# Kernel optimization log

Measured on AMD Instinct MI355X. Metric: run time of the kernel, lower is better.

Reference implementation:

```python
import jax, jax.numpy as jnp
import numpy as np

B = 64          # graphs per batch
N = 1500        # nodes per graph (equal sizes -> vectorized sortpool)
NT = B * N      # total nodes
DEG = 16        # avg in-degree
E_PER = N * DEG # edges per graph
F_IN = 128
K = 30          # sortpool k
LATENT = [32, 32, 32, 1]  # total 97
TOTAL_LAT = sum(LATENT)
OUT_DIM = 128


def setup_inputs() -> dict:
    key = jax.random.key(0)
    ks = jax.random.split(key, 16)
    node_feat = jax.random.normal(ks[0], (NT, F_IN), dtype=jnp.float32)
    # edges constrained within each graph (block-diagonal adjacency)
    offs = (jnp.arange(B, dtype=jnp.int32) * N)[:, None]
    edge_src = (jax.random.randint(ks[1], (B, E_PER), 0, N, dtype=jnp.int32) + offs).reshape(-1)
    edge_dst = (jax.random.randint(ks[2], (B, E_PER), 0, N, dtype=jnp.int32) + offs).reshape(-1)

    def lin(k, fan_in, shape):
        return jax.random.normal(k, shape, dtype=jnp.float32) * (1.0 / np.sqrt(fan_in))

    inp = dict(node_feat=node_feat, edge_src=edge_src, edge_dst=edge_dst)
    dims = [F_IN] + LATENT
    for i in range(4):
        inp[f'W{i+1}'] = lin(ks[3 + i], dims[i], (dims[i], dims[i + 1]))
        inp[f'b{i+1}'] = jnp.zeros((dims[i + 1],), jnp.float32)
    inp['conv1_w'] = lin(ks[8], TOTAL_LAT, (16, TOTAL_LAT))   # Conv1d(1,16,97,stride=97)
    inp['conv1_b'] = jnp.zeros((16,), jnp.float32)
    inp['conv2_w'] = lin(ks[9], 16 * 5, (32, 16, 5))          # Conv1d(16,32,5)
    inp['conv2_b'] = jnp.zeros((32,), jnp.float32)
    inp['out_w'] = lin(ks[10], 352, (352, OUT_DIM))
    inp['out_b'] = jnp.zeros((OUT_DIM,), jnp.float32)
    return inp


def reference(node_feat, edge_src, edge_dst, W1, b1, W2, b2, W3, b3, W4, b4,
              conv1_w, conv1_b, conv2_w, conv2_b, out_w, out_b):
    # node degrees (+1 for self loop), from in-edges
    deg = jax.ops.segment_sum(jnp.ones_like(edge_dst, jnp.float32), edge_dst, num_segments=NT)
    node_degs = (deg + 1.0)[:, None]

    # 4 graph-conv layers: (A @ h + h) -> Linear -> /deg -> tanh, concat features
    h = node_feat
    layers = []
    for W, b in ((W1, b1), (W2, b2), (W3, b3), (W4, b4)):
        agg = jax.ops.segment_sum(h[edge_src], edge_dst, num_segments=NT) + h
        h = jnp.tanh((agg @ W + b) / node_degs)
        layers.append(h)
    feat = jnp.concatenate(layers, axis=1)  # [NT, 97]

    # sortpooling: top-k nodes per graph by the last channel
    sort_ch = feat[:, -1].reshape(B, N)
    _, idx = jax.lax.top_k(sort_ch, K)                    # [B, K]
    gidx = (idx + (jnp.arange(B, dtype=idx.dtype) * N)[:, None]).reshape(-1)
    pooled = feat[gidx].reshape(B, K, TOTAL_LAT)          # [B, K, 97]

    # Conv1d(1,16,97,stride=97) over flattened [B,1,K*97] == per-slot linear
    c1 = jax.nn.relu(jnp.einsum('bkd,od->bok', pooled, conv1_w) + conv1_b[None, :, None])  # [B,16,K]
    mp = c1.reshape(B, 16, K // 2, 2).max(axis=-1)        # MaxPool1d(2,2) -> [B,16,15]
    c2 = jax.lax.conv_general_dilated(mp, conv2_w, (1,), 'VALID',
                                      dimension_numbers=('NCH', 'OIH', 'NCH'))
    c2 = jax.nn.relu(c2 + conv2_b[None, :, None])         # [B,32,11]
    dense = c2.reshape(B, -1)                             # [B,352]
    return jax.nn.relu(dense @ out_w + out_b)             # relu(relu(x)) == relu(x)
```

## Files before the change

### kernel.cpp

```cpp
#include <hip/hip_runtime.h>

constexpr int B = 64, N = 1500, NT = B * N;
constexpr int E_PER = 24000, E_TOT = B * E_PER;
constexpr int E_PAD = 28512;
constexpr int F_INN = 128, K = 30, TOT = 97;
constexpr int NB_G = 47;

__global__ __launch_bounds__(1024) void build_csr(const int* __restrict__ src, const int* __restrict__ dst,
                                                  int* __restrict__ csr, int* __restrict__ rowst,
                                                  int* __restrict__ degi, float* __restrict__ degf,
                                                  float* __restrict__ tA, float* __restrict__ tB,
                                                  float* __restrict__ t4) {
    __shared__ int hist[N];
    __shared__ int csr_l[E_PAD];
    __shared__ int wsum[4];
    int g = blockIdx.x, t = threadIdx.x;
    int gbase = g * N;
    const int* dstg = dst + (size_t)g * E_PER;
    const int* srcg = src + (size_t)g * E_PER;

    if (g == 0) {
        if (t < 32) tA[(size_t)NT * 32 + t] = 0.f;
        else if (t < 64) tB[(size_t)NT * 32 + (t - 32)] = 0.f;
        else if (t == 64) t4[NT] = 0.f;
    }

    for (int i = t; i < N; i += 1024) hist[i] = 0;
    for (int i = t; i < E_PAD; i += 1024) csr_l[i] = NT;
    __syncthreads();
    for (int e = t; e < E_PER; e += 1024)
        atomicAdd(&hist[dstg[e] - gbase], 1);
    __syncthreads();

    int local[6];
    int sum = 0, x = 0;
    if (t < 256) {
#pragma unroll
        for (int i = 0; i < 6; ++i) {
            int v = t * 6 + i;
            int d = (v < N) ? hist[v] : 0;
            local[i] = d;
            sum += (d + 3) & ~3;
        }
        x = sum;
        int lane = t & 63;
#pragma unroll
        for (int m = 1; m < 64; m <<= 1) {
            int y = __shfl_up(x, m, 64);
            if (lane >= m) x += y;
        }
        if (lane == 63) wsum[t >> 6] = x;
    }
    __syncthreads();
    if (t < 256) {
        int woff = 0;
        int wv = t >> 6;
        for (int w = 0; w < wv; ++w) woff += wsum[w];
        int run = x - sum + woff;
#pragma unroll
        for (int i = 0; i < 6; ++i) {
            int v = t * 6 + i;
            if (v < N) {
                rowst[gbase + v] = g * E_PAD + run;
                degi[gbase + v] = local[i];
                degf[gbase + v] = (float)(local[i] + 1);
                hist[v] = run;
                run += (local[i] + 3) & ~3;
            }
        }
    }
    __syncthreads();
    for (int e = t; e < E_PER; e += 1024) {
        int d = dstg[e] - gbase;
        int pos = atomicAdd(&hist[d], 1);
        csr_l[pos] = srcg[e];
    }
    __syncthreads();
    for (int i = t; i < E_PAD; i += 1024)
        csr[(size_t)g * E_PAD + i] = csr_l[i];
}

template <int KDIM>
__global__ __launch_bounds__(256) void gemm_t(const float* __restrict__ h,
                                              const float* __restrict__ W,
                                              float* __restrict__ t) {
    __shared__ float hs[32][128];
    __shared__ float Ws[32][32];
    int tid = threadIdx.x;
    int wv = tid >> 6, lane = tid & 63;
    int v0 = blockIdx.x * 128;
    int og = wv * 8;
    float acc[2][8];
#pragma unroll
    for (int i = 0; i < 2; ++i)
#pragma unroll
        for (int j = 0; j < 8; ++j) acc[i][j] = 0.f;

    for (int kc = 0; kc < KDIM; kc += 32) {
        __syncthreads();
        {
            int n = tid >> 1, kh = (tid & 1) * 16;
            const float* hp = h + (size_t)(v0 + n) * KDIM + kc + kh;
            const float4* hp4 = reinterpret_cast<const float4*>(hp);
            float4 a = hp4[0], b = hp4[1], c = hp4[2], d = hp4[3];
            hs[kh + 0][n] = a.x;  hs[kh + 1][n] = a.y;  hs[kh + 2][n] = a.z;  hs[kh + 3][n] = a.w;
            hs[kh + 4][n] = b.x;  hs[kh + 5][n] = b.y;  hs[kh + 6][n] = b.z;  hs[kh + 7][n] = b.w;
            hs[kh + 8][n] = c.x;  hs[kh + 9][n] = c.y;  hs[kh + 10][n] = c.z; hs[kh + 11][n] = c.w;
            hs[kh + 12][n] = d.x; hs[kh + 13][n] = d.y; hs[kh + 14][n] = d.z; hs[kh + 15][n] = d.w;
        }
        {
            int r = tid >> 3, c4 = (tid & 7) * 4;
            float4 w = *reinterpret_cast<const float4*>(W + (size_t)(kc + r) * 32 + c4);
            *reinterpret_cast<float4*>(&Ws[r][c4]) = w;
        }
        __syncthreads();
#pragma unroll
        for (int k = 0; k < 32; ++k) {
            float2 hv = *reinterpret_cast<const float2*>(&hs[k][2 * lane]);
            float4 w0 = *reinterpret_cast<const float4*>(&Ws[k][og]);
            float4 w1 = *reinterpret_cast<const float4*>(&Ws[k][og + 4]);
            acc[0][0] += hv.x * w0.x; acc[0][1] += hv.x * w0.y; acc[0][2] += hv.x * w0.z; acc[0][3] += hv.x * w0.w;
            acc[0][4] += hv.x * w1.x; acc[0][5] += hv.x * w1.y; acc[0][6] += hv.x * w1.z; acc[0][7] += hv.x * w1.w;
            acc[1][0] += hv.y * w0.x; acc[1][1] += hv.y * w0.y; acc[1][2] += hv.y * w0.z; acc[1][3] += hv.y * w0.w;
            acc[1][4] += hv.y * w1.x; acc[1][5] += hv.y * w1.y; acc[1][6] += hv.y * w1.z; acc[1][7] += hv.y * w1.w;
        }
    }
#pragma unroll
    for (int i = 0; i < 2; ++i) {
        float* op = t + (size_t)(v0 + 2 * lane + i) * 32 + og;
        float4 r0 = {acc[i][0], acc[i][1], acc[i][2], acc[i][3]};
        float4 r1 = {acc[i][4], acc[i][5], acc[i][6], acc[i][7]};
        reinterpret_cast<float4*>(op)[0] = r0;
        reinterpret_cast<float4*>(op)[1] = r1;
    }
}

template <int FUSE>
__global__ __launch_bounds__(256) void agg_f(const float* __restrict__ t,
                                             const int* __restrict__ csr, const int* __restrict__ rowst,
                                             const int* __restrict__ degi, const float* __restrict__ degf,
                                             const float* __restrict__ bias, const float* __restrict__ Wn,
                                             float* __restrict__ hout, float* __restrict__ tn) {
    __shared__ float Ws[1024];
    __shared__ float outs[32][32];
    if (FUSE == 32) {
        for (int i = threadIdx.x; i < 1024; i += 256) Ws[i] = Wn[i];
    }
    int bid = blockIdx.x;
    int xcd = bid & 7, j = bid >> 3;
    int g = xcd + 8 * (j / NB_G);
    int nb = j % NB_G;
    int nl = threadIdx.x >> 3;
    int f4 = threadIdx.x & 7;
    int vl = nb * 32 + nl;
    bool valid = vl < N;
    int v = g * N + vl;
    const float4* t4v = reinterpret_cast<const float4*>(t);
    float4 out = {0.f, 0.f, 0.f, 0.f};
    if (valid) {
        float4 acc = t4v[(unsigned)(v * 8 + f4)];
        int e0 = rowst[v];
        int dc = degi[v];
        int pc = (dc + 3) & ~3;
        float4 s1 = {0.f, 0.f, 0.f, 0.f}, s2 = {0.f, 0.f, 0.f, 0.f};
        for (int e = 0; e < pc; e += 4) {
            int4 s4 = *reinterpret_cast<const int4*>(csr + e0 + e);
            float4 x0 = t4v[(unsigned)(s4.x * 8 + f4)];
            float4 x1 = t4v[(unsigned)(s4.y * 8 + f4)];
            float4 x2 = t4v[(unsigned)(s4.z * 8 + f4)];
            float4 x3 = t4v[(unsigned)(s4.w * 8 + f4)];
            s1.x += x0.x + x1.x; s1.y += x0.y + x1.y; s1.z += x0.z + x1.z; s1.w += x0.w + x1.w;
            s2.x += x2.x + x3.x; s2.y += x2.y + x3.y; s2.z += x2.z + x3.z; s2.w += x2.w + x3.w;
        }
        acc.x += s1.x + s2.x; acc.y += s1.y + s2.y; acc.z += s1.z + s2.z; acc.w += s1.w + s2.w;
        float4 bv = *reinterpret_cast<const float4*>(bias + f4 * 4);
        float inv = 1.0f / degf[v];
        out.x = tanhf((acc.x + bv.x) * inv);
        out.y = tanhf((acc.y + bv.y) * inv);
        out.z = tanhf((acc.z + bv.z) * inv);
        out.w = tanhf((acc.w + bv.w) * inv);
        reinterpret_cast<float4*>(hout)[(unsigned)(v * 8 + f4)] = out;
    }
    if (FUSE == 32) {
        *reinterpret_cast<float4*>(&outs[nl][f4 * 4]) = out;
        __syncthreads();
        if (valid) {
            float4 s = {0.f, 0.f, 0.f, 0.f};
#pragma unroll
            for (int ff = 0; ff < 32; ++ff) {
                float h = outs[nl][ff];
                float4 wr = *reinterpret_cast<const float4*>(&Ws[ff * 32 + f4 * 4]);
                s.x += h * wr.x; s.y += h * wr.y; s.z += h * wr.z; s.w += h * wr.w;
            }
            reinterpret_cast<float4*>(tn)[(unsigned)(v * 8 + f4)] = s;
        }
    } else if (valid) {
        float4 w4 = *reinterpret_cast<const float4*>(Wn + f4 * 4);
        float p = out.x * w4.x + out.y * w4.y + out.z * w4.z + out.w * w4.w;
        p += __shfl_xor(p, 4, 64);
        p += __shfl_xor(p, 2, 64);
        p += __shfl_xor(p, 1, 64);
        if (f4 == 0) tn[v] = p;
    }
}

__global__ __launch_bounds__(256) void agg1f(const float* __restrict__ t4,
                                             const int* __restrict__ csr, const int* __restrict__ rowst,
                                             const int* __restrict__ degi, const float* __restrict__ degf,
                                             const float* __restrict__ b4, float* __restrict__ h4) {
    int v = blockIdx.x * 256 + threadIdx.x;
    if (v >= NT) return;
    float acc = t4[v];
    int e0 = rowst[v], dc = degi[v];
    int pc = (dc + 3) & ~3;
    float a0 = 0.f, a1 = 0.f, a2 = 0.f, a3 = 0.f;
    for (int e = 0; e < pc; e += 4) {
        int4 s4 = *reinterpret_cast<const int4*>(csr + e0 + e);
        a0 += t4[s4.x];
        a1 += t4[s4.y];
        a2 += t4[s4.z];
        a3 += t4[s4.w];
    }
    acc += (a0 + a1) + (a2 + a3);
    h4[v] = tanhf((acc + b4[0]) / degf[v]);
}

__global__ __launch_bounds__(512) void sort_head(const float* __restrict__ hc1, const float* __restrict__ hc2,
                                                 const float* __restrict__ hc3, const float* __restrict__ h4,
                                                 const float* __restrict__ c1w, const float* __restrict__ c1b,
                                                 const float* __restrict__ c2w, const float* __restrict__ c2b,
                                                 const float* __restrict__ ow, const float* __restrict__ ob,
                                                 float* __restrict__ out) {
    __shared__ unsigned int svals[N];
    __shared__ float fvals[N];
    __shared__ int hist[2048];
    __shared__ int canA[N], canB[N];
    __shared__ int winners[32];
    __shared__ int wsum[8];
    __shared__ int st_need, st_ncand, st_tb, st_cab, st_nwin;
    __shared__ int topk_s[K];
    __shared__ float pooled[K][TOT];
    __shared__ float c1[16][K];
    __shared__ float mp[16][16];
    __shared__ float dense[352];
    __shared__ float part[4][128];

    int g = blockIdx.x, t = threadIdx.x;
    int gbase = g * N;
    int lane = t & 63, w = t >> 6;

    for (int v = t; v < N; v += 512) {
        float f = h4[gbase + v];
        fvals[v] = f;
        unsigned int b = __float_as_uint(f);
        svals[v] = (b & 0x80000000u) ? ~b : (b | 0x80000000u);
    }
    if (t == 0) { st_need = K; st_nwin = 0; }

    auto mkkey = [&](int idx) {
        return ((unsigned long long)svals[idx] << 31) | (unsigned int)(0x7FFFFFFF - idx);
    };

    const int SHIFTS[6] = {52, 41, 30, 19, 8, 0};
    int curN = N;
    int src = 0;
    for (int pass = 0; pass < 6; ++pass) {
        int shift = SHIFTS[pass];
        int mask = (pass == 5) ? 0xFF : 0x7FF;
        for (int i = t; i < 2048; i += 512) hist[i] = 0;
        if (t == 0) st_ncand = 0;
        __syncthreads();
        for (int i = t; i < curN; i += 512) {
            int idx = (src == 0) ? i : (src == 1 ? canA[i] : canB[i]);
            int d = (int)((mkkey(idx) >> shift) & mask);
            atomicAdd(&hist[d], 1);
        }
        __syncthreads();
        int need = st_need;
        int c[4];
        int s = 0;
#pragma unroll
        for (int u = 0; u < 4; ++u) { c[u] = hist[2047 - (4 * t + u)]; s += c[u]; }
        int x = s;
#pragma unroll
        for (int m = 1; m < 64; m <<= 1) {
            int y = __shfl_up(x, m, 64);
            if (lane >= m) x += y;
        }
        if (lane == 63) wsum[w] = x;
        __syncthreads();
        int woff = 0;
        for (int ww = 0; ww < w; ++ww) woff += wsum[ww];
        int A = woff + x - s;
#pragma unroll
        for (int u = 0; u < 4; ++u) {
            if (A < need && need <= A + c[u]) { st_tb = 2047 - (4 * t + u); st_cab = A; }
            A += c[u];
        }
        __syncthreads();
        int tb = st_tb, cab = st_cab;
        int* dst = (src == 1) ? canB : canA;
        for (int i = t; i < curN; i += 512) {
            int idx = (src == 0) ? i : (src == 1 ? canA[i] : canB[i]);
            int d = (int)((mkkey(idx) >> shift) & mask);
            if (d > tb) {
                int p = atomicAdd(&st_nwin, 1);
                winners[p] = idx;
            } else if (d == tb) {
                int p = atomicAdd(&st_ncand, 1);
                dst[p] = idx;
            }
        }
        __syncthreads();
        int ncand = st_ncand;
        need -= cab;
        if (t == 0) st_need = need;
        if (ncand == need) {
            int base = st_nwin;
            for (int i = t; i < ncand; i += 512) winners[base + i] = dst[i];
            __syncthreads();
            break;
        }
        curN = ncand;
        src = (src == 1) ? 2 : 1;
        __syncthreads();
    }

    if (t < 64) {
        unsigned long long key = (t < K) ? mkkey(winners[t]) : 0ull;
        unsigned long long kk = ~key;
#pragma unroll
        for (int k = 2; k <= 64; k <<= 1) {
#pragma unroll
            for (int j = k >> 1; j > 0; j >>= 1) {
                unsigned long long o = __shfl_xor(kk, j, 64);
                bool keepMin = ((t & j) == 0) == ((t & k) == 0);
                kk = keepMin ? (kk < o ? kk : o) : (kk > o ? kk : o);
            }
        }
        key = ~kk;
        if (t < K) topk_s[t] = 0x7FFFFFFF - (int)(unsigned int)(key & 0x7FFFFFFFu);
    }
    __syncthreads();

    for (int i = t; i < K * TOT; i += 512) {
        int k = i / TOT, d = i % TOT;
        int vloc = topk_s[k];
        int gi = gbase + vloc;
        float val = (d < 32) ? hc1[(size_t)gi * 32 + d]
                  : (d < 64) ? hc2[(size_t)gi * 32 + d - 32]
                  : (d < 96) ? hc3[(size_t)gi * 32 + d - 64]
                             : fvals[vloc];
        pooled[k][d] = val;
    }
    __syncthreads();
    for (int i = t; i < 16 * K; i += 512) {
        int o = i / K, k = i % K;
        float s = c1b[o];
        for (int d = 0; d < TOT; ++d) s += pooled[k][d] * c1w[o * TOT + d];
        c1[o][k] = fmaxf(s, 0.f);
    }
    __syncthreads();
    for (int i = t; i < 16 * 15; i += 512) {
        int o = i / 15, p = i % 15;
        mp[o][p] = fmaxf(c1[o][2 * p], c1[o][2 * p + 1]);
    }
    __syncthreads();
    for (int i = t; i < 352; i += 512) {
        int o = i / 11, p = i % 11;
        float s = c2b[o];
#pragma unroll
        for (int ci = 0; ci < 16; ++ci)
#pragma unroll
            for (int tt = 0; tt < 5; ++tt)
                s += mp[ci][p + tt] * c2w[(o * 16 + ci) * 5 + tt];
        dense[i] = fmaxf(s, 0.f);
    }
    __syncthreads();
    {
        int o = t & 127, q = t >> 7;
        float s = 0.f;
        for (int m = q * 88; m < (q + 1) * 88; ++m) s += dense[m] * ow[m * 128 + o];
        part[q][o] = s;
    }
    __syncthreads();
    if (t < 128) {
        float s = (part[0][t] + part[1][t]) + (part[2][t] + part[3][t]) + ob[t];
        out[g * 128 + t] = fmaxf(s, 0.f);
    }
}

extern "C" void kernel_launch(void* const* d_in, const int* in_sizes, int n_in,
                              void* d_out, int out_size, void* d_ws, size_t ws_size,
                              hipStream_t stream) {
    const float* node_feat = (const float*)d_in[0];
    const int* esrc = (const int*)d_in[1];
    const int* edst = (const int*)d_in[2];
    const float* W1 = (const float*)d_in[3];
    const float* b1 = (const float*)d_in[4];
    const float* W2 = (const float*)d_in[5];
    const float* b2 = (const float*)d_in[6];
    const float* W3 = (const float*)d_in[7];
    const float* b3 = (const float*)d_in[8];
    const float* W4 = (const float*)d_in[9];
    const float* b4 = (const float*)d_in[10];
    const float* c1w = (const float*)d_in[11];
    const float* c1b = (const float*)d_in[12];
    const float* c2w = (const float*)d_in[13];
    const float* c2b = (const float*)d_in[14];
    const float* ow = (const float*)d_in[15];
    const float* ob = (const float*)d_in[16];

    char* ws = (char*)d_ws;
    size_t off = 0;
    auto alloc = [&](size_t bytes) {
        size_t r = off;
        off += (bytes + 255) & ~(size_t)255;
        return r;
    };
    int* deg_i = (int*)(ws + alloc((size_t)NT * 4));
    int* rowst = (int*)(ws + alloc((size_t)NT * 4));
    float* degf = (float*)(ws + alloc((size_t)NT * 4));
    int* csr = (int*)(ws + alloc((size_t)B * E_PAD * 4));
    float* tA = (float*)(ws + alloc((size_t)(NT + 1) * 32 * 4));
    float* tB = (float*)(ws + alloc((size_t)(NT + 1) * 32 * 4));
    float* hc1 = (float*)(ws + alloc((size_t)NT * 32 * 4));
    float* hc2 = (float*)(ws + alloc((size_t)NT * 32 * 4));
    float* hc3 = (float*)(ws + alloc((size_t)NT * 32 * 4));
    float* t4 = (float*)(ws + alloc((size_t)(NT + 1) * 4));
    float* h4 = (float*)(ws + alloc((size_t)NT * 4));

    build_csr<<<B, 1024, 0, stream>>>(esrc, edst, csr, rowst, deg_i, degf, tA, tB, t4);

    gemm_t<F_INN><<<NT / 128, 256, 0, stream>>>(node_feat, W1, tA);
    agg_f<32><<<8 * NB_G * 8, 256, 0, stream>>>(tA, csr, rowst, deg_i, degf, b1, W2, hc1, tB);
    agg_f<32><<<8 * NB_G * 8, 256, 0, stream>>>(tB, csr, rowst, deg_i, degf, b2, W3, hc2, tA);
    agg_f<1><<<8 * NB_G * 8, 256, 0, stream>>>(tA, csr, rowst, deg_i, degf, b3, W4, hc3, t4);
    agg1f<<<(NT + 255) / 256, 256, 0, stream>>>(t4, csr, rowst, deg_i, degf, b4, h4);

    sort_head<<<B, 512, 0, stream>>>(hc1, hc2, hc3, h4, c1w, c1b, c2w, c2b, ow, ob, (float*)d_out);
}
```

Before: 127.7 us.

## Split CSR construction across four node-quarter blocks per graph

build_csr now launches four blocks per graph instead of one. Each block owns a quarter of the destination nodes and builds its own histogram, scan and CSR slice in a smaller shared buffer (CAP=8192). The goal is to fill more of the GPU, since 64 blocks leave most CUs idle, and to cut per-block LDS use. In exchange, every block reads the full edge list of its graph, so edge reads go up fourfold. A quarter whose padded edge count exceeds CAP would overflow, though random inputs stay well below that.

```diff
diff --git a/kernel.cpp b/kernel.cpp
--- a/kernel.cpp
+++ b/kernel.cpp
@@ -2,7 +2,8 @@
 
 constexpr int B = 64, N = 1500, NT = B * N;
 constexpr int E_PER = 24000, E_TOT = B * E_PER;
-constexpr int E_PAD = 28512;
+constexpr int NQ = 4, NPQ = N / NQ;
+constexpr int CAP = 8192;
 constexpr int F_INN = 128, K = 30, TOT = 97;
 constexpr int NB_G = 47;
 
@@ -11,34 +12,38 @@
                                                   int* __restrict__ degi, float* __restrict__ degf,
                                                   float* __restrict__ tA, float* __restrict__ tB,
                                                   float* __restrict__ t4) {
-    __shared__ int hist[N];
-    __shared__ int csr_l[E_PAD];
-    __shared__ int wsum[4];
-    int g = blockIdx.x, t = threadIdx.x;
-    int gbase = g * N;
+    __shared__ int hist[NPQ];
+    __shared__ int csr_l[CAP];
+    __shared__ int wtot;
+    int bid = blockIdx.x;
+    int g = bid >> 2, q = bid & 3;
+    int t = threadIdx.x;
+    int gbase = g * N, qlo = q * NPQ;
     const int* dstg = dst + (size_t)g * E_PER;
     const int* srcg = src + (size_t)g * E_PER;
 
-    if (g == 0) {
+    if (bid == 0) {
         if (t < 32) tA[(size_t)NT * 32 + t] = 0.f;
         else if (t < 64) tB[(size_t)NT * 32 + (t - 32)] = 0.f;
         else if (t == 64) t4[NT] = 0.f;
     }
 
-    for (int i = t; i < N; i += 1024) hist[i] = 0;
-    for (int i = t; i < E_PAD; i += 1024) csr_l[i] = NT;
-    __syncthreads();
-    for (int e = t; e < E_PER; e += 1024)
-        atomicAdd(&hist[dstg[e] - gbase], 1);
-    __syncthreads();
-
-    int local[6];
+    for (int i = t; i < NPQ; i += 1024) hist[i] = 0;
+    for (int i = t; i < CAP; i += 1024) csr_l[i] = NT;
+    __syncthreads();
+    for (int e = t; e < E_PER; e += 1024) {
+        int d = dstg[e] - gbase - qlo;
+        if ((unsigned)d < (unsigned)NPQ) atomicAdd(&hist[d], 1);
+    }
+    __syncthreads();
+
+    int local[3];
     int sum = 0, x = 0;
-    if (t < 256) {
-#pragma unroll
-        for (int i = 0; i < 6; ++i) {
-            int v = t * 6 + i;
-            int d = (v < N) ? hist[v] : 0;
+    if (t < 128) {
+#pragma unroll
+        for (int i = 0; i < 3; ++i) {
+            int v = t * 3 + i;
+            int d = (v < NPQ) ? hist[v] : 0;
             local[i] = d;
             sum += (d + 3) & ~3;
         }
@@ -49,21 +54,20 @@
             int y = __shfl_up(x, m, 64);
             if (lane >= m) x += y;
         }
-        if (lane == 63) wsum[t >> 6] = x;
-    }
-    __syncthreads();
-    if (t < 256) {
-        int woff = 0;
-        int wv = t >> 6;
-        for (int w = 0; w < wv; ++w) woff += wsum[w];
-        int run = x - sum + woff;
-#pragma unroll
-        for (int i = 0; i < 6; ++i) {
-            int v = t * 6 + i;
-            if (v < N) {
-                rowst[gbase + v] = g * E_PAD + run;
-                degi[gbase + v] = local[i];
-                degf[gbase + v] = (float)(local[i] + 1);
+    }
+    if (t == 63) wtot = x;
+    __syncthreads();
+    if (t < 128) {
+        int base = (t >= 64) ? wtot : 0;
+        int run = base + x - sum;
+        int rbase = (g * NQ + q) * CAP;
+#pragma unroll
+        for (int i = 0; i < 3; ++i) {
+            int v = t * 3 + i;
+            if (v < NPQ) {
+                rowst[gbase + qlo + v] = rbase + run;
+                degi[gbase + qlo + v] = local[i];
+                degf[gbase + qlo + v] = (float)(local[i] + 1);
                 hist[v] = run;
                 run += (local[i] + 3) & ~3;
             }
@@ -71,13 +75,16 @@
     }
     __syncthreads();
     for (int e = t; e < E_PER; e += 1024) {
-        int d = dstg[e] - gbase;
-        int pos = atomicAdd(&hist[d], 1);
-        csr_l[pos] = srcg[e];
-    }
-    __syncthreads();
-    for (int i = t; i < E_PAD; i += 1024)
-        csr[(size_t)g * E_PAD + i] = csr_l[i];
+        int d = dstg[e] - gbase - qlo;
+        if ((unsigned)d < (unsigned)NPQ) {
+            int pos = atomicAdd(&hist[d], 1);
+            csr_l[pos] = srcg[e];
+        }
+    }
+    __syncthreads();
+    int* cg = csr + (size_t)(g * NQ + q) * CAP;
+    for (int i = t; i < CAP; i += 1024)
+        cg[i] = csr_l[i];
 }
 
 template <int KDIM>
@@ -421,7 +428,7 @@
     int* deg_i = (int*)(ws + alloc((size_t)NT * 4));
     int* rowst = (int*)(ws + alloc((size_t)NT * 4));
     float* degf = (float*)(ws + alloc((size_t)NT * 4));
-    int* csr = (int*)(ws + alloc((size_t)B * E_PAD * 4));
+    int* csr = (int*)(ws + alloc((size_t)B * NQ * CAP * 4));
     float* tA = (float*)(ws + alloc((size_t)(NT + 1) * 32 * 4));
     float* tB = (float*)(ws + alloc((size_t)(NT + 1) * 32 * 4));
     float* hc1 = (float*)(ws + alloc((size_t)NT * 32 * 4));
@@ -430,7 +437,7 @@
     float* t4 = (float*)(ws + alloc((size_t)(NT + 1) * 4));
     float* h4 = (float*)(ws + alloc((size_t)NT * 4));
 
-    build_csr<<<B, 1024, 0, stream>>>(esrc, edst, csr, rowst, deg_i, degf, tA, tB, t4);
+    build_csr<<<B * NQ, 1024, 0, stream>>>(esrc, edst, csr, rowst, deg_i, degf, tA, tB, t4);
 
     gemm_t<F_INN><<<NT / 128, 256, 0, stream>>>(node_feat, W1, tA);
     agg_f<32><<<8 * NB_G * 8, 256, 0, stream>>>(tA, csr, rowst, deg_i, degf, b1, W2, hc1, tB);
```

After: 129.8 us. Within noise of the previous version (+1.7%).

## Merge CSR build with first GEMM and fold last aggregation into sort_head

Applied to the files above, without the earlier changes.

Merges the CSR-building kernel and the first dense GEMM into one launch: the first B blocks build the CSR, and the remaining blocks each run four 128-node GEMM tiles in a shared-memory union. It also removes the separate scalar layer-4 aggregation kernel. sort_head now stages each graph's t4 values in LDS, gathers neighbours from there and applies tanh inline. This saves two launches and the h4 round trip through global memory. The cost is a large LDS footprint in prep, which limits occupancy for the GEMM blocks, and only 64 blocks doing the layer-4 gather.

```diff
diff --git a/kernel.cpp b/kernel.cpp
--- a/kernel.cpp
+++ b/kernel.cpp
@@ -5,133 +5,139 @@
 constexpr int E_PAD = 28512;
 constexpr int F_INN = 128, K = 30, TOT = 97;
 constexpr int NB_G = 47;
-
-__global__ __launch_bounds__(1024) void build_csr(const int* __restrict__ src, const int* __restrict__ dst,
-                                                  int* __restrict__ csr, int* __restrict__ rowst,
-                                                  int* __restrict__ degi, float* __restrict__ degf,
-                                                  float* __restrict__ tA, float* __restrict__ tB,
-                                                  float* __restrict__ t4) {
-    __shared__ int hist[N];
-    __shared__ int csr_l[E_PAD];
-    __shared__ int wsum[4];
-    int g = blockIdx.x, t = threadIdx.x;
-    int gbase = g * N;
-    const int* dstg = dst + (size_t)g * E_PER;
-    const int* srcg = src + (size_t)g * E_PER;
-
-    if (g == 0) {
-        if (t < 32) tA[(size_t)NT * 32 + t] = 0.f;
-        else if (t < 64) tB[(size_t)NT * 32 + (t - 32)] = 0.f;
-        else if (t == 64) t4[NT] = 0.f;
-    }
-
-    for (int i = t; i < N; i += 1024) hist[i] = 0;
-    for (int i = t; i < E_PAD; i += 1024) csr_l[i] = NT;
-    __syncthreads();
-    for (int e = t; e < E_PER; e += 1024)
-        atomicAdd(&hist[dstg[e] - gbase], 1);
-    __syncthreads();
-
-    int local[6];
-    int sum = 0, x = 0;
-    if (t < 256) {
-#pragma unroll
-        for (int i = 0; i < 6; ++i) {
-            int v = t * 6 + i;
-            int d = (v < N) ? hist[v] : 0;
-            local[i] = d;
-            sum += (d + 3) & ~3;
-        }
-        x = sum;
-        int lane = t & 63;
-#pragma unroll
-        for (int m = 1; m < 64; m <<= 1) {
-            int y = __shfl_up(x, m, 64);
-            if (lane >= m) x += y;
-        }
-        if (lane == 63) wsum[t >> 6] = x;
-    }
-    __syncthreads();
-    if (t < 256) {
-        int woff = 0;
-        int wv = t >> 6;
-        for (int w = 0; w < wv; ++w) woff += wsum[w];
-        int run = x - sum + woff;
-#pragma unroll
-        for (int i = 0; i < 6; ++i) {
-            int v = t * 6 + i;
-            if (v < N) {
-                rowst[gbase + v] = g * E_PAD + run;
-                degi[gbase + v] = local[i];
-                degf[gbase + v] = (float)(local[i] + 1);
-                hist[v] = run;
-                run += (local[i] + 3) & ~3;
-            }
-        }
-    }
-    __syncthreads();
-    for (int e = t; e < E_PER; e += 1024) {
-        int d = dstg[e] - gbase;
-        int pos = atomicAdd(&hist[d], 1);
-        csr_l[pos] = srcg[e];
-    }
-    __syncthreads();
-    for (int i = t; i < E_PAD; i += 1024)
-        csr[(size_t)g * E_PAD + i] = csr_l[i];
-}
-
-template <int KDIM>
-__global__ __launch_bounds__(256) void gemm_t(const float* __restrict__ h,
-                                              const float* __restrict__ W,
-                                              float* __restrict__ t) {
-    __shared__ float hs[32][128];
-    __shared__ float Ws[32][32];
-    int tid = threadIdx.x;
-    int wv = tid >> 6, lane = tid & 63;
-    int v0 = blockIdx.x * 128;
-    int og = wv * 8;
-    float acc[2][8];
-#pragma unroll
-    for (int i = 0; i < 2; ++i)
-#pragma unroll
-        for (int j = 0; j < 8; ++j) acc[i][j] = 0.f;
-
-    for (int kc = 0; kc < KDIM; kc += 32) {
-        __syncthreads();
-        {
-            int n = tid >> 1, kh = (tid & 1) * 16;
-            const float* hp = h + (size_t)(v0 + n) * KDIM + kc + kh;
-            const float4* hp4 = reinterpret_cast<const float4*>(hp);
-            float4 a = hp4[0], b = hp4[1], c = hp4[2], d = hp4[3];
-            hs[kh + 0][n] = a.x;  hs[kh + 1][n] = a.y;  hs[kh + 2][n] = a.z;  hs[kh + 3][n] = a.w;
-            hs[kh + 4][n] = b.x;  hs[kh + 5][n] = b.y;  hs[kh + 6][n] = b.z;  hs[kh + 7][n] = b.w;
-            hs[kh + 8][n] = c.x;  hs[kh + 9][n] = c.y;  hs[kh + 10][n] = c.z; hs[kh + 11][n] = c.w;
-            hs[kh + 12][n] = d.x; hs[kh + 13][n] = d.y; hs[kh + 14][n] = d.z; hs[kh + 15][n] = d.w;
-        }
-        {
-            int r = tid >> 3, c4 = (tid & 7) * 4;
-            float4 w = *reinterpret_cast<const float4*>(W + (size_t)(kc + r) * 32 + c4);
-            *reinterpret_cast<float4*>(&Ws[r][c4]) = w;
-        }
-        __syncthreads();
-#pragma unroll
-        for (int k = 0; k < 32; ++k) {
-            float2 hv = *reinterpret_cast<const float2*>(&hs[k][2 * lane]);
-            float4 w0 = *reinterpret_cast<const float4*>(&Ws[k][og]);
-            float4 w1 = *reinterpret_cast<const float4*>(&Ws[k][og + 4]);
-            acc[0][0] += hv.x * w0.x; acc[0][1] += hv.x * w0.y; acc[0][2] += hv.x * w0.z; acc[0][3] += hv.x * w0.w;
-            acc[0][4] += hv.x * w1.x; acc[0][5] += hv.x * w1.y; acc[0][6] += hv.x * w1.z; acc[0][7] += hv.x * w1.w;
-            acc[1][0] += hv.y * w0.x; acc[1][1] += hv.y * w0.y; acc[1][2] += hv.y * w0.z; acc[1][3] += hv.y * w0.w;
-            acc[1][4] += hv.y * w1.x; acc[1][5] += hv.y * w1.y; acc[1][6] += hv.y * w1.z; acc[1][7] += hv.y * w1.w;
-        }
-    }
-#pragma unroll
-    for (int i = 0; i < 2; ++i) {
-        float* op = t + (size_t)(v0 + 2 * lane + i) * 32 + og;
-        float4 r0 = {acc[i][0], acc[i][1], acc[i][2], acc[i][3]};
-        float4 r1 = {acc[i][4], acc[i][5], acc[i][6], acc[i][7]};
-        reinterpret_cast<float4*>(op)[0] = r0;
-        reinterpret_cast<float4*>(op)[1] = r1;
+constexpr int GEMM_TILES = NT / 128;
+constexpr int GEMM_BLKS = (GEMM_TILES + 3) / 4;
+
+__global__ __launch_bounds__(1024) void prep(const int* __restrict__ src, const int* __restrict__ dst,
+                                             int* __restrict__ csr, int* __restrict__ rowst,
+                                             int* __restrict__ degi, float* __restrict__ degf,
+                                             float* __restrict__ tA, float* __restrict__ tB,
+                                             float* __restrict__ t4,
+                                             const float* __restrict__ nf, const float* __restrict__ W1) {
+    __shared__ union {
+        struct { int hist[N]; int csr_l[E_PAD]; int wsum[4]; } c;
+        struct { float hs[4][32][128]; float Ws[4][32][32]; } g;
+    } u;
+    int bid = blockIdx.x, t = threadIdx.x;
+
+    if (bid < B) {
+        int g = bid;
+        int gbase = g * N;
+        const int* dstg = dst + (size_t)g * E_PER;
+        const int* srcg = src + (size_t)g * E_PER;
+
+        if (g == 0) {
+            if (t < 32) tA[(size_t)NT * 32 + t] = 0.f;
+            else if (t < 64) tB[(size_t)NT * 32 + (t - 32)] = 0.f;
+            else if (t == 64) t4[NT] = 0.f;
+        }
+
+        for (int i = t; i < N; i += 1024) u.c.hist[i] = 0;
+        for (int i = t; i < E_PAD; i += 1024) u.c.csr_l[i] = NT;
+        __syncthreads();
+        for (int e = t; e < E_PER; e += 1024)
+            atomicAdd(&u.c.hist[dstg[e] - gbase], 1);
+        __syncthreads();
+
+        int local[6];
+        int sum = 0, x = 0;
+        if (t < 256) {
+#pragma unroll
+            for (int i = 0; i < 6; ++i) {
+                int v = t * 6 + i;
+                int d = (v < N) ? u.c.hist[v] : 0;
+                local[i] = d;
+                sum += (d + 3) & ~3;
+            }
+            x = sum;
+            int lane = t & 63;
+#pragma unroll
+            for (int m = 1; m < 64; m <<= 1) {
+                int y = __shfl_up(x, m, 64);
+                if (lane >= m) x += y;
+            }
+            if (lane == 63) u.c.wsum[t >> 6] = x;
+        }
+        __syncthreads();
+        if (t < 256) {
+            int woff = 0;
+            int wv = t >> 6;
+            for (int w = 0; w < wv; ++w) woff += u.c.wsum[w];
+            int run = x - sum + woff;
+#pragma unroll
+            for (int i = 0; i < 6; ++i) {
+                int v = t * 6 + i;
+                if (v < N) {
+                    rowst[gbase + v] = g * E_PAD + run;
+                    degi[gbase + v] = local[i];
+                    degf[gbase + v] = (float)(local[i] + 1);
+                    u.c.hist[v] = run;
+                    run += (local[i] + 3) & ~3;
+                }
+            }
+        }
+        __syncthreads();
+        for (int e = t; e < E_PER; e += 1024) {
+            int d = dstg[e] - gbase;
+            int pos = atomicAdd(&u.c.hist[d], 1);
+            u.c.csr_l[pos] = srcg[e];
+        }
+        __syncthreads();
+        for (int i = t; i < E_PAD; i += 1024)
+            csr[(size_t)g * E_PAD + i] = u.c.csr_l[i];
+    } else {
+        int sub = t >> 8, tid = t & 255;
+        int tile = (bid - B) * 4 + sub;
+        bool valid = tile < GEMM_TILES;
+        int wv = tid >> 6, lane = tid & 63;
+        int v0 = tile * 128;
+        int og = wv * 8;
+        float acc[2][8];
+#pragma unroll
+        for (int i = 0; i < 2; ++i)
+#pragma unroll
+            for (int j = 0; j < 8; ++j) acc[i][j] = 0.f;
+
+        for (int kc = 0; kc < F_INN; kc += 32) {
+            __syncthreads();
+            if (valid) {
+                int n = tid >> 1, kh = (tid & 1) * 16;
+                const float* hp = nf + (size_t)(v0 + n) * F_INN + kc + kh;
+                const float4* hp4 = reinterpret_cast<const float4*>(hp);
+                float4 a = hp4[0], b = hp4[1], c = hp4[2], d = hp4[3];
+                float (*hs)[128] = u.g.hs[sub];
+                hs[kh + 0][n] = a.x;  hs[kh + 1][n] = a.y;  hs[kh + 2][n] = a.z;  hs[kh + 3][n] = a.w;
+                hs[kh + 4][n] = b.x;  hs[kh + 5][n] = b.y;  hs[kh + 6][n] = b.z;  hs[kh + 7][n] = b.w;
+                hs[kh + 8][n] = c.x;  hs[kh + 9][n] = c.y;  hs[kh + 10][n] = c.z; hs[kh + 11][n] = c.w;
+                hs[kh + 12][n] = d.x; hs[kh + 13][n] = d.y; hs[kh + 14][n] = d.z; hs[kh + 15][n] = d.w;
+                int r = tid >> 3, c4 = (tid & 7) * 4;
+                float4 w = *reinterpret_cast<const float4*>(W1 + (size_t)(kc + r) * 32 + c4);
+                *reinterpret_cast<float4*>(&u.g.Ws[sub][r][c4]) = w;
+            }
+            __syncthreads();
+            if (valid) {
+#pragma unroll
+                for (int k = 0; k < 32; ++k) {
+                    float2 hv = *reinterpret_cast<const float2*>(&u.g.hs[sub][k][2 * lane]);
+                    float4 w0 = *reinterpret_cast<const float4*>(&u.g.Ws[sub][k][og]);
+                    float4 w1 = *reinterpret_cast<const float4*>(&u.g.Ws[sub][k][og + 4]);
+                    acc[0][0] += hv.x * w0.x; acc[0][1] += hv.x * w0.y; acc[0][2] += hv.x * w0.z; acc[0][3] += hv.x * w0.w;
+                    acc[0][4] += hv.x * w1.x; acc[0][5] += hv.x * w1.y; acc[0][6] += hv.x * w1.z; acc[0][7] += hv.x * w1.w;
+                    acc[1][0] += hv.y * w0.x; acc[1][1] += hv.y * w0.y; acc[1][2] += hv.y * w0.z; acc[1][3] += hv.y * w0.w;
+                    acc[1][4] += hv.y * w1.x; acc[1][5] += hv.y * w1.y; acc[1][6] += hv.y * w1.z; acc[1][7] += hv.y * w1.w;
+                }
+            }
+        }
+        if (valid) {
+#pragma unroll
+            for (int i = 0; i < 2; ++i) {
+                float* op = tA + (size_t)(v0 + 2 * lane + i) * 32 + og;
+                float4 r0 = {acc[i][0], acc[i][1], acc[i][2], acc[i][3]};
+                float4 r1 = {acc[i][4], acc[i][5], acc[i][6], acc[i][7]};
+                reinterpret_cast<float4*>(op)[0] = r0;
+                reinterpret_cast<float4*>(op)[1] = r1;
+            }
+        }
     }
 }
 
@@ -204,33 +210,16 @@
     }
 }
 
-__global__ __launch_bounds__(256) void agg1f(const float* __restrict__ t4,
-                                             const int* __restrict__ csr, const int* __restrict__ rowst,
-                                             const int* __restrict__ degi, const float* __restrict__ degf,
-                                             const float* __restrict__ b4, float* __restrict__ h4) {
-    int v = blockIdx.x * 256 + threadIdx.x;
-    if (v >= NT) return;
-    float acc = t4[v];
-    int e0 = rowst[v], dc = degi[v];
-    int pc = (dc + 3) & ~3;
-    float a0 = 0.f, a1 = 0.f, a2 = 0.f, a3 = 0.f;
-    for (int e = 0; e < pc; e += 4) {
-        int4 s4 = *reinterpret_cast<const int4*>(csr + e0 + e);
-        a0 += t4[s4.x];
-        a1 += t4[s4.y];
-        a2 += t4[s4.z];
-        a3 += t4[s4.w];
-    }
-    acc += (a0 + a1) + (a2 + a3);
-    h4[v] = tanhf((acc + b4[0]) / degf[v]);
-}
-
 __global__ __launch_bounds__(512) void sort_head(const float* __restrict__ hc1, const float* __restrict__ hc2,
-                                                 const float* __restrict__ hc3, const float* __restrict__ h4,
+                                                 const float* __restrict__ hc3, const float* __restrict__ t4,
+                                                 const int* __restrict__ csr, const int* __restrict__ rowst,
+                                                 const int* __restrict__ degi, const float* __restrict__ degf,
+                                                 const float* __restrict__ b4,
                                                  const float* __restrict__ c1w, const float* __restrict__ c1b,
                                                  const float* __restrict__ c2w, const float* __restrict__ c2b,
                                                  const float* __restrict__ ow, const float* __restrict__ ob,
                                                  float* __restrict__ out) {
+    __shared__ float ts[N + 1];
     __shared__ unsigned int svals[N];
     __shared__ float fvals[N];
     __shared__ int hist[2048];
@@ -249,13 +238,35 @@
     int gbase = g * N;
     int lane = t & 63, w = t >> 6;
 
-    for (int v = t; v < N; v += 512) {
-        float f = h4[gbase + v];
-        fvals[v] = f;
-        unsigned int b = __float_as_uint(f);
-        svals[v] = (b & 0x80000000u) ? ~b : (b | 0x80000000u);
-    }
-    if (t == 0) { st_need = K; st_nwin = 0; }
+    for (int v = t; v < N; v += 512) ts[v] = t4[gbase + v];
+    if (t == 0) ts[N] = 0.f;
+    if (t == 1) { st_need = K; st_nwin = 0; }
+    __syncthreads();
+    {
+        float b4v = b4[0];
+        for (int v = t; v < N; v += 512) {
+            int gv = gbase + v;
+            int e0 = rowst[gv], dc = degi[gv];
+            int pc = (dc + 3) & ~3;
+            float a0 = 0.f, a1 = 0.f, a2 = 0.f, a3 = 0.f;
+            for (int e = 0; e < pc; e += 4) {
+                int4 s4 = *reinterpret_cast<const int4*>(csr + e0 + e);
+                unsigned l0 = min((unsigned)(s4.x - gbase), (unsigned)N);
+                unsigned l1 = min((unsigned)(s4.y - gbase), (unsigned)N);
+                unsigned l2 = min((unsigned)(s4.z - gbase), (unsigned)N);
+                unsigned l3 = min((unsigned)(s4.w - gbase), (unsigned)N);
+                a0 += ts[l0];
+                a1 += ts[l1];
+                a2 += ts[l2];
+                a3 += ts[l3];
+            }
+            float h = tanhf((ts[v] + (a0 + a1) + (a2 + a3) + b4v) / degf[gv]);
+            fvals[v] = h;
+            unsigned int b = __float_as_uint(h);
+            svals[v] = (b & 0x80000000u) ? ~b : (b | 0x80000000u);
+        }
+    }
+    __syncthreads();
 
     auto mkkey = [&](int idx) {
         return ((unsigned long long)svals[idx] << 31) | (unsigned int)(0x7FFFFFFF - idx);
@@ -428,15 +439,14 @@
     float* hc2 = (float*)(ws + alloc((size_t)NT * 32 * 4));
     float* hc3 = (float*)(ws + alloc((size_t)NT * 32 * 4));
     float* t4 = (float*)(ws + alloc((size_t)(NT + 1) * 4));
-    float* h4 = (float*)(ws + alloc((size_t)NT * 4));
-
-    build_csr<<<B, 1024, 0, stream>>>(esrc, edst, csr, rowst, deg_i, degf, tA, tB, t4);
-
-    gemm_t<F_INN><<<NT / 128, 256, 0, stream>>>(node_feat, W1, tA);
+
+    prep<<<B + GEMM_BLKS, 1024, 0, stream>>>(esrc, edst, csr, rowst, deg_i, degf,
+                                             tA, tB, t4, node_feat, W1);
+
     agg_f<32><<<8 * NB_G * 8, 256, 0, stream>>>(tA, csr, rowst, deg_i, degf, b1, W2, hc1, tB);
     agg_f<32><<<8 * NB_G * 8, 256, 0, stream>>>(tB, csr, rowst, deg_i, degf, b2, W3, hc2, tA);
     agg_f<1><<<8 * NB_G * 8, 256, 0, stream>>>(tA, csr, rowst, deg_i, degf, b3, W4, hc3, t4);
-    agg1f<<<(NT + 255) / 256, 256, 0, stream>>>(t4, csr, rowst, deg_i, degf, b4, h4);
-
-    sort_head<<<B, 512, 0, stream>>>(hc1, hc2, hc3, h4, c1w, c1b, c2w, c2b, ow, ob, (float*)d_out);
+
+    sort_head<<<B, 512, 0, stream>>>(hc1, hc2, hc3, t4, csr, rowst, deg_i, degf, b4,
+                                     c1w, c1b, c2w, c2b, ow, ob, (float*)d_out);
 }
```

After: 120.2 us. -5.9%, faster.
